# Performance work log

Hardware: AMD Instinct MI355X
Metric: run time of the kernel (lower is better)

Reference implementation:

```python
import jax, jax.numpy as jnp
import numpy as np

T, N, F_IND, F_MAC = 250, 4000, 46, 178
H = 64
F_IN = F_IND + F_MAC  # dense-net input = firm chars + tiled macro = 224


def setup_inputs() -> dict:
    key = jax.random.key(0)
    ks = jax.random.split(key, 9)
    macro_features = jax.random.normal(ks[0], (1, T, F_MAC), jnp.float32)
    individual_features = jax.random.normal(ks[1], (1, T, N, F_IND), jnp.float32)
    masks = jnp.ones((1, T, N, 1), dtype=bool)
    returns_tensor = jax.random.normal(ks[2], (1, T, N, 1), jnp.float32) * 0.05
    W1 = jax.random.normal(ks[3], (F_IN, H), jnp.float32) / np.sqrt(F_IN).astype(np.float32)
    b1 = jnp.zeros((H,), jnp.float32)
    W2 = jax.random.normal(ks[4], (H, H), jnp.float32) / np.sqrt(H).astype(np.float32)
    b2 = jnp.zeros((H,), jnp.float32)
    W3 = jax.random.normal(ks[5], (H, 1), jnp.float32) / np.sqrt(H).astype(np.float32)
    b3 = jnp.zeros((1,), jnp.float32)
    return {"macro_features": macro_features, "individual_features": individual_features,
            "masks": masks, "returns_tensor": returns_tensor,
            "W1": W1, "b1": b1, "W2": W2, "b2": b2, "W3": W3, "b3": b3}


def reference(macro_features, individual_features, masks, returns_tensor, W1, b1, W2, b2, W3, b3):
    B, Tt, Nn, _ = individual_features.shape
    # tile macro state over assets and concat with firm characteristics -> [1,T,N,F_IN]
    mac = jnp.broadcast_to(macro_features[:, :, None, :], (B, Tt, Nn, macro_features.shape[-1]))
    dense_inputs = jnp.concatenate([individual_features, mac], axis=-1)
    mf = masks.astype(dense_inputs.dtype)  # [1,T,N,1]
    # dense net: 2 relu hidden layers + linear head, output_size=1 (SDF weight per firm-month)
    h = jax.nn.relu(dense_inputs @ W1 + b1)
    h = jax.nn.relu(h @ W2 + b2)
    weights = (h @ W3 + b3) * mf  # zero out masked entries (mask is all-ones -> static shape)
    # weighted returns and per-time segment sum (== torch.split + per-segment torch.sum)
    weighted_returns = returns_tensor * weights * mf
    num_val_per_time = jnp.sum(mf[0, :, :, 0], axis=1)  # [T]
    sum_per_time = jnp.sum(weighted_returns[0, :, :, 0], axis=1)  # [T]
    # normalize_w = True
    sum_per_time = sum_per_time / num_val_per_time * jnp.mean(num_val_per_time)
    sdf = (sum_per_time + 1.0)[:, None]  # [T,1]
    weights_flat = weights.reshape(1, Tt * Nn, 1)  # matches masked_select layout (all-true mask)
    return sdf, weights_flat
```

## Files before the change

kernel.cpp:

```cpp
#include <hip/hip_runtime.h>

#define T_DIM 250
#define N_DIM 4000
#define F_IND 46
#define F_MAC 178
#define H_DIM 64

typedef __bf16         bf16x8  __attribute__((ext_vector_type(8)));
typedef float          f32x4   __attribute__((ext_vector_type(4)));
typedef unsigned short ushort8 __attribute__((ext_vector_type(8)));

union FragU { ushort8 u; bf16x8 b; };

__device__ __forceinline__ unsigned short f2bf(float f) {
    unsigned u = __float_as_uint(f);
    return (unsigned short)((u + 0x7fffu + ((u >> 16) & 1u)) >> 16);
}
__device__ __forceinline__ unsigned pack2bf(float lo, float hi) {
    return (unsigned)f2bf(lo) | ((unsigned)f2bf(hi) << 16);
}

__global__ __launch_bounds__(256)
void prep_kernel(const float* __restrict__ mac,
                 const float* __restrict__ W1,
                 const float* __restrict__ b1,
                 const float* __restrict__ W2,
                 unsigned short* __restrict__ Wb1,
                 unsigned short* __restrict__ Wb2,
                 float* __restrict__ Mproj,
                 float* __restrict__ sdf)
{
    const int b = blockIdx.x;
    const int tid = threadIdx.x;
    if (b < 2) {
        const float* W = (b == 0) ? W1 : W2;
        unsigned short* dst = (b == 0) ? Wb1 : Wb2;
        const int kmax = (b == 0) ? F_IND : H_DIM;
        for (int idx = tid; idx < 4096; idx += 256) {
            int j  = idx & 7;
            int L  = (idx >> 3) & 63;
            int rt = (idx >> 9) & 3;
            int s  = idx >> 11;
            int k  = s * 32 + ((L >> 4) * 8) + j;
            int c  = rt * 16 + (L & 15);
            float v = (k < kmax) ? W[k * H_DIM + c] : 0.0f;
            dst[idx] = f2bf(v);
        }
    } else {
        __shared__ float red[4][H_DIM];
        const int t  = b - 2;
        const int j  = tid & 63;
        const int kc = tid >> 6;
        const int k0 = kc * 45;
        const int k1 = (k0 + 45 < F_MAC) ? k0 + 45 : F_MAC;
        float acc = (kc == 0) ? b1[j] : 0.0f;
        const float* mrow = mac + t * F_MAC;
        for (int k = k0; k < k1; ++k)
            acc = fmaf(mrow[k], W1[(F_IND + k) * H_DIM + j], acc);
        red[kc][j] = acc;
        __syncthreads();
        if (tid < 64) {
            Mproj[t * H_DIM + j] = red[0][j] + red[1][j] + red[2][j] + red[3][j];
            if (tid == 0) sdf[t] = 1.0f;
        }
    }
}

__global__ __launch_bounds__(256)
void mlp_mfma(const float* __restrict__ ind,
              const float* __restrict__ ret,
              const unsigned short* __restrict__ Wb1,
              const unsigned short* __restrict__ Wb2,
              const float* __restrict__ Mproj,
              const float* __restrict__ b2,
              const float* __restrict__ W3,
              const float* __restrict__ b3,
              float* __restrict__ out_w,
              float* __restrict__ sdf)
{
    __shared__ unsigned Xsh[256 * 32];

    const int tid  = threadIdx.x;
    const int lane = tid & 63;
    const int w    = tid >> 6;
    const int q    = lane >> 4;
    const int m    = lane & 15;
    const int m7   = m & 7;
    const int t    = blockIdx.y;
    const int n0   = blockIdx.x * 256;
    const int rbase = w * 64;
    const int nwave = n0 + rbase;

    const int  nlane = nwave + lane;
    const bool lval  = nlane < N_DIM;
    float retv = 0.0f;
    if (lval) retv = ret[(size_t)t * N_DIM + nlane];

    FragU a1[2][4];
    #pragma unroll
    for (int s = 0; s < 2; ++s)
        #pragma unroll
        for (int rt = 0; rt < 4; ++rt)
            a1[s][rt].u = *(const ushort8*)(Wb1 + ((s * 4 + rt) * 64 + lane) * 8);

    f32x4 mp[4];
    #pragma unroll
    for (int rt = 0; rt < 4; ++rt)
        mp[rt] = *(const f32x4*)(Mproj + t * H_DIM + rt * 16 + q * 4);

    {
        const float2* tf2 = (const float2*)(ind + ((size_t)t * N_DIM + nwave) * F_IND);
        unsigned* base = Xsh + rbase * 32;
        const int c2  = lane & 31;
        const int slb = lane >> 5;
        const bool full = (nwave + 64 <= N_DIM);

        if (full) {
            #pragma unroll
            for (int ch = 0; ch < 2; ++ch) {
                float2 v[16];
                #pragma unroll
                for (int i = 0; i < 16; ++i) {
                    int it = ch * 16 + i;
                    v[i] = (c2 < 23) ? tf2[(it * 2 + slb) * 23 + c2]
                                     : float2{0.0f, 0.0f};
                }
                #pragma unroll
                for (int i = 0; i < 16; ++i) {
                    int it = ch * 16 + i;
                    int sl = it * 2 + slb;
                    base[sl * 32 + (c2 ^ ((sl & 7) << 2))] = pack2bf(v[i].x, v[i].y);
                }
            }
        } else {
            #pragma unroll
            for (int it = 0; it < 32; ++it) {
                int sl = it * 2 + slb;
                unsigned dw = 0;
                if (c2 < 23 && (nwave + sl) < N_DIM) {
                    float2 v = tf2[sl * 23 + c2];
                    dw = pack2bf(v.x, v.y);
                }
                base[sl * 32 + (c2 ^ ((sl & 7) << 2))] = dw;
            }
        }
    }

    f32x4 acc[4][4];
    #pragma unroll
    for (int rt = 0; rt < 4; ++rt)
        #pragma unroll
        for (int ct = 0; ct < 4; ++ct)
            acc[rt][ct] = mp[rt];

    #pragma unroll
    for (int s = 0; s < 2; ++s) {
        FragU xf[4];
        #pragma unroll
        for (int ct = 0; ct < 4; ++ct) {
            int sl  = ct * 16 + m;
            int blk = (s * 4 + q) ^ m7;
            xf[ct].u = *(const ushort8*)(Xsh + (rbase + sl) * 32 + blk * 4);
        }
        #pragma unroll
        for (int rt = 0; rt < 4; ++rt)
            #pragma unroll
            for (int ct = 0; ct < 4; ++ct)
                acc[rt][ct] = __builtin_amdgcn_mfma_f32_16x16x32_bf16(
                    a1[s][rt].b, xf[ct].b, acc[rt][ct], 0, 0, 0);
    }

    FragU a2[2][4];
    #pragma unroll
    for (int s = 0; s < 2; ++s)
        #pragma unroll
        for (int rt = 0; rt < 4; ++rt)
            a2[s][rt].u = *(const ushort8*)(Wb2 + ((s * 4 + rt) * 64 + lane) * 8);

    f32x4 bb2[4];
    #pragma unroll
    for (int rt = 0; rt < 4; ++rt)
        bb2[rt] = *(const f32x4*)(b2 + rt * 16 + q * 4);

    #pragma unroll
    for (int rt = 0; rt < 4; ++rt)
        #pragma unroll
        for (int ct = 0; ct < 4; ++ct) {
            int sl = ct * 16 + m;
            unsigned lo = pack2bf(fmaxf(acc[rt][ct][0], 0.0f),
                                  fmaxf(acc[rt][ct][1], 0.0f));
            unsigned hi = pack2bf(fmaxf(acc[rt][ct][2], 0.0f),
                                  fmaxf(acc[rt][ct][3], 0.0f));
            int phys = ((rt * 2 + (q >> 1)) ^ m7) * 4 + (q & 1) * 2;
            uint2 v; v.x = lo; v.y = hi;
            *(uint2*)(Xsh + (rbase + sl) * 32 + phys) = v;
        }

    f32x4 acc2[4][4];
    #pragma unroll
    for (int rt = 0; rt < 4; ++rt)
        #pragma unroll
        for (int ct = 0; ct < 4; ++ct)
            acc2[rt][ct] = bb2[rt];

    #pragma unroll
    for (int s = 0; s < 2; ++s) {
        FragU hf[4];
        #pragma unroll
        for (int ct = 0; ct < 4; ++ct) {
            int sl  = ct * 16 + m;
            int blk = (s * 4 + q) ^ m7;
            hf[ct].u = *(const ushort8*)(Xsh + (rbase + sl) * 32 + blk * 4);
        }
        #pragma unroll
        for (int rt = 0; rt < 4; ++rt)
            #pragma unroll
            for (int ct = 0; ct < 4; ++ct)
                acc2[rt][ct] = __builtin_amdgcn_mfma_f32_16x16x32_bf16(
                    a2[s][rt].b, hf[ct].b, acc2[rt][ct], 0, 0, 0);
    }

    float wv;
    {
        f32x4 w3[4];
        #pragma unroll
        for (int rt = 0; rt < 4; ++rt)
            w3[rt] = *(const f32x4*)(W3 + rt * 16 + q * 4);
        const float b3s = b3[0];

        float pq[4];
        #pragma unroll
        for (int ct = 0; ct < 4; ++ct) {
            float p = 0.0f;
            #pragma unroll
            for (int rt = 0; rt < 4; ++rt)
                #pragma unroll
                for (int r = 0; r < 4; ++r)
                    p = fmaf(fmaxf(acc2[rt][ct][r], 0.0f), w3[rt][r], p);
            p += __shfl_xor(p, 16, 64);
            p += __shfl_xor(p, 32, 64);
            pq[ct] = p;
        }
        wv = (q == 0) ? pq[0] : (q == 1) ? pq[1] : (q == 2) ? pq[2] : pq[3];
        wv += b3s;
    }

    float contrib = 0.0f;
    if (lval) {
        out_w[(size_t)t * N_DIM + nlane] = wv;
        contrib = retv * wv;
    }
    #pragma unroll
    for (int off = 32; off > 0; off >>= 1)
        contrib += __shfl_down(contrib, off, 64);
    if (lane == 0) atomicAdd(&sdf[t], contrib);
}

extern "C" void kernel_launch(void* const* d_in, const int* in_sizes, int n_in,
                              void* d_out, int out_size, void* d_ws, size_t ws_size,
                              hipStream_t stream) {
    (void)in_sizes; (void)n_in; (void)out_size; (void)ws_size;

    const float* mac = (const float*)d_in[0];
    const float* ind = (const float*)d_in[1];
    const float* ret = (const float*)d_in[3];
    const float* W1  = (const float*)d_in[4];
    const float* b1  = (const float*)d_in[5];
    const float* W2  = (const float*)d_in[6];
    const float* b2  = (const float*)d_in[7];
    const float* W3  = (const float*)d_in[8];
    const float* b3  = (const float*)d_in[9];

    float* sdf   = (float*)d_out;
    float* out_w = (float*)d_out + T_DIM;

    unsigned short* Wb1 = (unsigned short*)d_ws;
    unsigned short* Wb2 = Wb1 + 4096;
    float* Mproj = (float*)((char*)d_ws + 16384);

    prep_kernel<<<dim3(252), 256, 0, stream>>>(mac, W1, b1, W2, Wb1, Wb2, Mproj, sdf);

    dim3 grid((N_DIM + 255) / 256, T_DIM);
    mlp_mfma<<<grid, 256, 0, stream>>>(ind, ret, Wb1, Wb2, Mproj, b2, W3, b3,
                                       out_w, sdf);
}
```

Before: 333.2 us.

## Load layer-1 input fragments directly from global into MFMA registers, skip LDS staging

Each lane now loads its fp32 input features from global memory straight into registers in the MFMA B-fragment layout and converts them to bf16 in place, instead of staging the tile through shared memory. The second K-step (features 32-45) is loaded only by the quads that hold real data and is zero-filled elsewhere. The layer-2 accumulators reuse the layer-1 registers, the launch bounds ask for 3 blocks per CU, and the hand-written bf16 rounding is replaced by native __bf16 casts. This removes an LDS write/read round trip and its latency before the first matmul, at the cost of strided, poorly coalesced global loads (8-byte aligned float4 per row) and some lane imbalance between quads.

```diff
diff --git a/kernel.cpp b/kernel.cpp
--- a/kernel.cpp
+++ b/kernel.cpp
@@ -9,15 +9,17 @@
 typedef __bf16         bf16x8  __attribute__((ext_vector_type(8)));
 typedef float          f32x4   __attribute__((ext_vector_type(4)));
 typedef unsigned short ushort8 __attribute__((ext_vector_type(8)));
+typedef float          f32x4a8 __attribute__((ext_vector_type(4), aligned(8)));
 
 union FragU { ushort8 u; bf16x8 b; };
+union BF2   { unsigned u; __bf16 h[2]; };
 
 __device__ __forceinline__ unsigned short f2bf(float f) {
     unsigned u = __float_as_uint(f);
     return (unsigned short)((u + 0x7fffu + ((u >> 16) & 1u)) >> 16);
 }
-__device__ __forceinline__ unsigned pack2bf(float lo, float hi) {
-    return (unsigned)f2bf(lo) | ((unsigned)f2bf(hi) << 16);
+__device__ __forceinline__ unsigned packbf2(float lo, float hi) {
+    BF2 p; p.h[0] = (__bf16)lo; p.h[1] = (__bf16)hi; return p.u;
 }
 
 __global__ __launch_bounds__(256)
@@ -66,7 +68,7 @@
     }
 }
 
-__global__ __launch_bounds__(256)
+__global__ __launch_bounds__(256, 3)
 void mlp_mfma(const float* __restrict__ ind,
               const float* __restrict__ ret,
               const unsigned short* __restrict__ Wb1,
@@ -78,7 +80,7 @@
               float* __restrict__ out_w,
               float* __restrict__ sdf)
 {
-    __shared__ unsigned Xsh[256 * 32];
+    __shared__ unsigned Hsh[256 * 32];
 
     const int tid  = threadIdx.x;
     const int lane = tid & 63;
@@ -96,128 +98,148 @@
     float retv = 0.0f;
     if (lval) retv = ret[(size_t)t * N_DIM + nlane];
 
-    FragU a1[2][4];
+    const float* xr = ind + ((size_t)t * N_DIM + (nwave + m)) * F_IND;
+    const int CTS = 16 * F_IND;
+    const bool fullw = (nwave + 64 <= N_DIM);
+
+    const f32x4a8 z4 = {};
+
+    f32x4a8 xa[4], xb[4];
+    if (fullw) {
+        #pragma unroll
+        for (int ct = 0; ct < 4; ++ct) {
+            const float* p = xr + ct * CTS + q * 8;
+            xa[ct] = *(const f32x4a8*)(p);
+            xb[ct] = *(const f32x4a8*)(p + 4);
+        }
+    } else {
+        #pragma unroll
+        for (int ct = 0; ct < 4; ++ct) {
+            const float* p = xr + ct * CTS + q * 8;
+            if ((nwave + ct * 16 + m) < N_DIM) {
+                xa[ct] = *(const f32x4a8*)(p);
+                xb[ct] = *(const f32x4a8*)(p + 4);
+            } else { xa[ct] = z4; xb[ct] = z4; }
+        }
+    }
+
+    FragU a1s0[4];
+    #pragma unroll
+    for (int rt = 0; rt < 4; ++rt)
+        a1s0[rt].u = *(const ushort8*)(Wb1 + (rt * 64 + lane) * 8);
+    f32x4 mp[4];
+    #pragma unroll
+    for (int rt = 0; rt < 4; ++rt)
+        mp[rt] = *(const f32x4*)(Mproj + t * H_DIM + rt * 16 + q * 4);
+
+    FragU xf[4];
+    #pragma unroll
+    for (int ct = 0; ct < 4; ++ct)
+        #pragma unroll
+        for (int i = 0; i < 4; ++i) {
+            xf[ct].b[i]     = (__bf16)xa[ct][i];
+            xf[ct].b[i + 4] = (__bf16)xb[ct][i];
+        }
+
+    f32x4a8 ya[4] = {}, yb[4] = {};
+    if (q == 0) {
+        #pragma unroll
+        for (int ct = 0; ct < 4; ++ct)
+            if (fullw || (nwave + ct * 16 + m) < N_DIM) {
+                ya[ct] = *(const f32x4a8*)(xr + ct * CTS + 32);
+                yb[ct] = *(const f32x4a8*)(xr + ct * CTS + 36);
+            }
+    } else if (q == 1) {
+        #pragma unroll
+        for (int ct = 0; ct < 4; ++ct)
+            if (fullw || (nwave + ct * 16 + m) < N_DIM) {
+                ya[ct] = *(const f32x4a8*)(xr + ct * CTS + 40);
+                float2 z = *(const float2*)(xr + ct * CTS + 44);
+                yb[ct][0] = z.x; yb[ct][1] = z.y;
+            }
+    }
+
+    f32x4 acc[4][4];
+    #pragma unroll
+    for (int rt = 0; rt < 4; ++rt)
+        #pragma unroll
+        for (int ct = 0; ct < 4; ++ct)
+            acc[rt][ct] = mp[rt];
+
+    #pragma unroll
+    for (int rt = 0; rt < 4; ++rt)
+        #pragma unroll
+        for (int ct = 0; ct < 4; ++ct)
+            acc[rt][ct] = __builtin_amdgcn_mfma_f32_16x16x32_bf16(
+                a1s0[rt].b, xf[ct].b, acc[rt][ct], 0, 0, 0);
+
+    FragU a1s1[4];
+    #pragma unroll
+    for (int rt = 0; rt < 4; ++rt)
+        a1s1[rt].u = *(const ushort8*)(Wb1 + ((4 + rt) * 64 + lane) * 8);
+
+    FragU yf[4];
+    #pragma unroll
+    for (int ct = 0; ct < 4; ++ct)
+        #pragma unroll
+        for (int i = 0; i < 4; ++i) {
+            yf[ct].b[i]     = (__bf16)ya[ct][i];
+            yf[ct].b[i + 4] = (__bf16)yb[ct][i];
+        }
+
+    #pragma unroll
+    for (int rt = 0; rt < 4; ++rt)
+        #pragma unroll
+        for (int ct = 0; ct < 4; ++ct)
+            acc[rt][ct] = __builtin_amdgcn_mfma_f32_16x16x32_bf16(
+                a1s1[rt].b, yf[ct].b, acc[rt][ct], 0, 0, 0);
+
+    FragU a2[2][4];
     #pragma unroll
     for (int s = 0; s < 2; ++s)
         #pragma unroll
         for (int rt = 0; rt < 4; ++rt)
-            a1[s][rt].u = *(const ushort8*)(Wb1 + ((s * 4 + rt) * 64 + lane) * 8);
-
-    f32x4 mp[4];
-    #pragma unroll
-    for (int rt = 0; rt < 4; ++rt)
-        mp[rt] = *(const f32x4*)(Mproj + t * H_DIM + rt * 16 + q * 4);
-
-    {
-        const float2* tf2 = (const float2*)(ind + ((size_t)t * N_DIM + nwave) * F_IND);
-        unsigned* base = Xsh + rbase * 32;
-        const int c2  = lane & 31;
-        const int slb = lane >> 5;
-        const bool full = (nwave + 64 <= N_DIM);
-
-        if (full) {
-            #pragma unroll
-            for (int ch = 0; ch < 2; ++ch) {
-                float2 v[16];
-                #pragma unroll
-                for (int i = 0; i < 16; ++i) {
-                    int it = ch * 16 + i;
-                    v[i] = (c2 < 23) ? tf2[(it * 2 + slb) * 23 + c2]
-                                     : float2{0.0f, 0.0f};
-                }
-                #pragma unroll
-                for (int i = 0; i < 16; ++i) {
-                    int it = ch * 16 + i;
-                    int sl = it * 2 + slb;
-                    base[sl * 32 + (c2 ^ ((sl & 7) << 2))] = pack2bf(v[i].x, v[i].y);
-                }
-            }
-        } else {
-            #pragma unroll
-            for (int it = 0; it < 32; ++it) {
-                int sl = it * 2 + slb;
-                unsigned dw = 0;
-                if (c2 < 23 && (nwave + sl) < N_DIM) {
-                    float2 v = tf2[sl * 23 + c2];
-                    dw = pack2bf(v.x, v.y);
-                }
-                base[sl * 32 + (c2 ^ ((sl & 7) << 2))] = dw;
-            }
-        }
-    }
-
-    f32x4 acc[4][4];
-    #pragma unroll
-    for (int rt = 0; rt < 4; ++rt)
-        #pragma unroll
-        for (int ct = 0; ct < 4; ++ct)
-            acc[rt][ct] = mp[rt];
+            a2[s][rt].u = *(const ushort8*)(Wb2 + ((s * 4 + rt) * 64 + lane) * 8);
+    f32x4 bb2[4];
+    #pragma unroll
+    for (int rt = 0; rt < 4; ++rt)
+        bb2[rt] = *(const f32x4*)(b2 + rt * 16 + q * 4);
+
+    #pragma unroll
+    for (int rt = 0; rt < 4; ++rt)
+        #pragma unroll
+        for (int ct = 0; ct < 4; ++ct) {
+            int sl = ct * 16 + m;
+            unsigned lo = packbf2(fmaxf(acc[rt][ct][0], 0.0f),
+                                  fmaxf(acc[rt][ct][1], 0.0f));
+            unsigned hi = packbf2(fmaxf(acc[rt][ct][2], 0.0f),
+                                  fmaxf(acc[rt][ct][3], 0.0f));
+            int phys = ((rt * 2 + (q >> 1)) ^ m7) * 4 + (q & 1) * 2;
+            uint2 v; v.x = lo; v.y = hi;
+            *(uint2*)(Hsh + (rbase + sl) * 32 + phys) = v;
+        }
+
+    #pragma unroll
+    for (int rt = 0; rt < 4; ++rt)
+        #pragma unroll
+        for (int ct = 0; ct < 4; ++ct)
+            acc[rt][ct] = bb2[rt];
 
     #pragma unroll
     for (int s = 0; s < 2; ++s) {
-        FragU xf[4];
+        FragU hf[4];
         #pragma unroll
         for (int ct = 0; ct < 4; ++ct) {
             int sl  = ct * 16 + m;
             int blk = (s * 4 + q) ^ m7;
-            xf[ct].u = *(const ushort8*)(Xsh + (rbase + sl) * 32 + blk * 4);
+            hf[ct].u = *(const ushort8*)(Hsh + (rbase + sl) * 32 + blk * 4);
         }
         #pragma unroll
         for (int rt = 0; rt < 4; ++rt)
             #pragma unroll
             for (int ct = 0; ct < 4; ++ct)
                 acc[rt][ct] = __builtin_amdgcn_mfma_f32_16x16x32_bf16(
-                    a1[s][rt].b, xf[ct].b, acc[rt][ct], 0, 0, 0);
-    }
-
-    FragU a2[2][4];
-    #pragma unroll
-    for (int s = 0; s < 2; ++s)
-        #pragma unroll
-        for (int rt = 0; rt < 4; ++rt)
-            a2[s][rt].u = *(const ushort8*)(Wb2 + ((s * 4 + rt) * 64 + lane) * 8);
-
-    f32x4 bb2[4];
-    #pragma unroll
-    for (int rt = 0; rt < 4; ++rt)
-        bb2[rt] = *(const f32x4*)(b2 + rt * 16 + q * 4);
-
-    #pragma unroll
-    for (int rt = 0; rt < 4; ++rt)
-        #pragma unroll
-        for (int ct = 0; ct < 4; ++ct) {
-            int sl = ct * 16 + m;
-            unsigned lo = pack2bf(fmaxf(acc[rt][ct][0], 0.0f),
-                                  fmaxf(acc[rt][ct][1], 0.0f));
-            unsigned hi = pack2bf(fmaxf(acc[rt][ct][2], 0.0f),
-                                  fmaxf(acc[rt][ct][3], 0.0f));
-            int phys = ((rt * 2 + (q >> 1)) ^ m7) * 4 + (q & 1) * 2;
-            uint2 v; v.x = lo; v.y = hi;
-            *(uint2*)(Xsh + (rbase + sl) * 32 + phys) = v;
-        }
-
-    f32x4 acc2[4][4];
-    #pragma unroll
-    for (int rt = 0; rt < 4; ++rt)
-        #pragma unroll
-        for (int ct = 0; ct < 4; ++ct)
-            acc2[rt][ct] = bb2[rt];
-
-    #pragma unroll
-    for (int s = 0; s < 2; ++s) {
-        FragU hf[4];
-        #pragma unroll
-        for (int ct = 0; ct < 4; ++ct) {
-            int sl  = ct * 16 + m;
-            int blk = (s * 4 + q) ^ m7;
-            hf[ct].u = *(const ushort8*)(Xsh + (rbase + sl) * 32 + blk * 4);
-        }
-        #pragma unroll
-        for (int rt = 0; rt < 4; ++rt)
-            #pragma unroll
-            for (int ct = 0; ct < 4; ++ct)
-                acc2[rt][ct] = __builtin_amdgcn_mfma_f32_16x16x32_bf16(
-                    a2[s][rt].b, hf[ct].b, acc2[rt][ct], 0, 0, 0);
+                    a2[s][rt].b, hf[ct].b, acc[rt][ct], 0, 0, 0);
     }
 
     float wv;
@@ -236,7 +258,7 @@
             for (int rt = 0; rt < 4; ++rt)
                 #pragma unroll
                 for (int r = 0; r < 4; ++r)
-                    p = fmaf(fmaxf(acc2[rt][ct][r], 0.0f), w3[rt][r], p);
+                    p = fmaf(fmaxf(acc[rt][ct][r], 0.0f), w3[rt][r], p);
             p += __shfl_xor(p, 16, 64);
             p += __shfl_xor(p, 32, 64);
             pq[ct] = p;
```

After: 321.6 us. 1.04x faster.
